# Performance work log

Measured on AMD Instinct MI355X. Metric: run time of the kernel, lower is better.

The kernel has to match this reference:

```python
import jax, jax.numpy as jnp
import numpy as np

EMBED = 1024
HEADS = 16
HEAD_DIM = EMBED // HEADS
FFN_DIM = 4096
SEQ = 2048
BATCH = 2
EPS = 1e-5


def setup_inputs() -> dict:
    key = jax.random.key(0)
    ks = jax.random.split(key, 13)
    s = lambda n: 1.0 / np.sqrt(n)
    return {
        "x": jax.random.normal(ks[0], (BATCH, SEQ, EMBED), jnp.float32),
        # qkv projection (stored as [in, out])
        "w_qkv": jax.random.normal(ks[1], (EMBED, 3 * EMBED), jnp.float32) * s(EMBED),
        "b_qkv": jax.random.normal(ks[2], (3 * EMBED,), jnp.float32) * 0.02,
        "w_out": jax.random.normal(ks[3], (EMBED, EMBED), jnp.float32) * s(EMBED),
        "b_out": jax.random.normal(ks[4], (EMBED,), jnp.float32) * 0.02,
        # FFN
        "w_up": jax.random.normal(ks[5], (EMBED, FFN_DIM), jnp.float32) * s(EMBED),
        "b_up": jax.random.normal(ks[6], (FFN_DIM,), jnp.float32) * 0.02,
        "w_down": jax.random.normal(ks[7], (FFN_DIM, EMBED), jnp.float32) * s(FFN_DIM),
        "b_down": jax.random.normal(ks[8], (EMBED,), jnp.float32) * 0.02,
        # LayerNorms
        "g1": jnp.ones((EMBED,), jnp.float32),
        "be1": jnp.zeros((EMBED,), jnp.float32),
        "g2": jnp.ones((EMBED,), jnp.float32),
        "be2": jnp.zeros((EMBED,), jnp.float32),
    }


def _layernorm(x, g, b):
    mu = jnp.mean(x, axis=-1, keepdims=True)
    var = jnp.mean(jnp.square(x - mu), axis=-1, keepdims=True)
    return (x - mu) * jax.lax.rsqrt(var + EPS) * g + b


def reference(x, w_qkv, b_qkv, w_out, b_out, w_up, b_up, w_down, b_down, g1, be1, g2, be2):
    B, S, E = x.shape
    qkv = (x @ w_qkv + b_qkv).reshape(B, S, 3, HEADS, HEAD_DIM)
    qkv = jnp.transpose(qkv, (2, 0, 3, 1, 4))
    q, k, v = qkv[0], qkv[1], qkv[2]
    scale = 1.0 / jnp.sqrt(jnp.float32(HEAD_DIM))
    attn = jnp.einsum("bhqd,bhkd->bhqk", q, k) * scale  # [B,H,S,S]
    causal = jnp.tril(jnp.ones((S, S), bool))
    attn = jnp.where(causal, attn, -jnp.inf)
    attn = jax.nn.softmax(attn, axis=-1)
    out = jnp.einsum("bhqk,bhkd->bhqd", attn, v)  # [B,H,S,D]
    out = jnp.transpose(out, (0, 2, 1, 3)).reshape(B, S, E)
    attn_out = out @ w_out + b_out
    x = _layernorm(x + attn_out, g1, be1)
    ffn_out = jax.nn.relu(x @ w_up + b_up) @ w_down + b_down
    return _layernorm(x + ffn_out, g2, be2)
```

## Files before the change

kernel.cpp:

```cpp
#include <hip/hip_runtime.h>
#include <hip/hip_bf16.h>

#define EMBED 1024
#define HEADS 16
#define HDIM 64
#define FFN 4096
#define SEQ 2048
#define BATCH 2
#define MTOT (BATCH*SEQ)
#define QSCALE 0.1803368801111137f

typedef __attribute__((ext_vector_type(8))) short bf16x8;
typedef __attribute__((ext_vector_type(4))) float f32x4;
typedef __attribute__((ext_vector_type(16))) float f32x16;
typedef unsigned short u16;
typedef unsigned int u32;

__device__ __forceinline__ u16 f2bf(float f) {
  union { float f; unsigned u; } v; v.f = f;
  unsigned r = v.u + 0x7FFFu + ((v.u >> 16) & 1u);
  return (u16)(r >> 16);
}

__device__ __forceinline__ void async_ld16(const void* g, void* l) {
  __builtin_amdgcn_global_load_lds((const __attribute__((address_space(1))) void*)g,
                                   (__attribute__((address_space(3))) void*)l,
                                   16, 0, 0);
}

__device__ __forceinline__ void qkv_scatter(u16* qp, u16* kp, u16* vp,
                                            int row, int col, float v) {
  const int which = col >> 10, hh = (col >> 6) & 15, d = col & 63;
  const int bb = row >> 11, ss = row & 2047;
  const int bh = bb * 16 + hh;
  if (which == 0) {
    v *= QSCALE;
    size_t idx = ((((size_t)bh * 64 + (ss >> 5)) * 4 + (d >> 4)) << 9)
               + (((ss & 31) + 32 * ((d >> 3) & 1)) << 3) + (d & 7);
    qp[idx] = f2bf(v);
  } else if (which == 1) {
    size_t idx = ((((size_t)bh * 32 + (ss >> 6)) * 8 + (d >> 4) * 2 + ((ss >> 5) & 1)) << 9)
               + (((ss & 31) + 32 * ((d >> 3) & 1)) << 3) + (d & 7);
    kp[idx] = f2bf(v);
  } else {
    size_t idx = ((((size_t)bh * 32 + (ss >> 6)) * 8 + ((ss & 63) >> 4) * 2 + (d >> 5)) << 9)
               + (((d & 31) + 32 * ((ss >> 3) & 1)) << 3) + (ss & 7);
    vp[idx] = f2bf(v);
  }
}

__global__ __launch_bounds__(256) void k_cvt(const float* __restrict__ in,
                                             u16* __restrict__ out, int n4) {
  int i = blockIdx.x * 256 + threadIdx.x;
  int st = gridDim.x * 256;
  for (; i < n4; i += st) {
    float4 v = ((const float4*)in)[i];
    ushort4 o;
    o.x = f2bf(v.x); o.y = f2bf(v.y); o.z = f2bf(v.z); o.w = f2bf(v.w);
    ((ushort4*)out)[i] = o;
  }
}

__global__ __launch_bounds__(256) void k_tr(const float* __restrict__ w,
                                            u16* __restrict__ wT, int K, int N) {
  __shared__ u16 tile[32][33];
  int n0 = blockIdx.x * 32, k0 = blockIdx.y * 32;
  int tx = threadIdx.x, ty = threadIdx.y;
  #pragma unroll
  for (int i = 0; i < 4; ++i) {
    int k = k0 + ty + i * 8;
    tile[ty + i * 8][tx] = f2bf(w[(size_t)k * N + n0 + tx]);
  }
  __syncthreads();
  #pragma unroll
  for (int i = 0; i < 4; ++i) {
    int n = n0 + ty + i * 8;
    wT[(size_t)n * K + k0 + tx] = tile[tx][ty + i * 8];
  }
}

template <int OMODE, bool RELU>
__global__ __launch_bounds__(512) void k_gemm8(
    const u16* __restrict__ A, const u16* __restrict__ BT,
    const float* __restrict__ bias,
    void* __restrict__ out0, void* __restrict__ out1, void* __restrict__ out2,
    int M, int N, int K) {
  __shared__ __align__(16) u16 As[2][2][128 * 64];
  __shared__ __align__(16) u16 Bs[2][2][128 * 64];
  const int tid = threadIdx.x;
  const int lane = tid & 63, g = lane >> 4, li = lane & 15;
  const int wid = tid >> 6, wm = wid >> 2, wn = wid & 3;

  const int gx = gridDim.x;
  const int nwg = gx * gridDim.y;
  const int flat = blockIdx.y * gx + blockIdx.x;
  const int cpx = nwg >> 3;
  const int swz = (flat & 7) * cpx + (flat >> 3);
  const int m0 = (swz / gx) * 256, n0 = (swz % gx) * 256;

  f32x4 acc[8][4] = {};

  const u16* Ablk = A + (size_t)m0 * K;
  const u16* Bblk = BT + (size_t)n0 * K;
  const int trow = tid >> 3;
  const int sc = (tid & 7) ^ (trow & 7);

  auto stageA = [&](int buf, int h, int kt) {
    #pragma unroll
    for (int r = 0; r < 2; ++r)
      async_ld16(Ablk + (size_t)(h * 64 + r * 128 + trow) * K + kt + sc * 8,
                 &As[buf][h][0] + r * 4096 + tid * 8);
  };
  auto stageB = [&](int buf, int h, int kt) {
    #pragma unroll
    for (int r = 0; r < 2; ++r) {
      const int p = trow + r * 64;
      async_ld16(Bblk + (size_t)(((p >> 5) << 6) + h * 32 + (p & 31)) * K + kt + sc * 8,
                 &Bs[buf][h][0] + r * 4096 + tid * 8);
    }
  };

#define VM4_ asm volatile("s_waitcnt vmcnt(4)" ::: "memory")
#define VM2_ asm volatile("s_waitcnt vmcnt(2)" ::: "memory")
#define VM0_ asm volatile("s_waitcnt vmcnt(0)" ::: "memory")
#define VMN_
#define GP8(IH, JH, VMSTMT, STAGE_STMT) do {                                   \
    bf16x8 a_[4][2], b_[2][2];                                                 \
    _Pragma("unroll")                                                          \
    for (int i2 = 0; i2 < 4; ++i2) {                                           \
      const int pa = wm * 64 + i2 * 16 + li;                                   \
      _Pragma("unroll")                                                        \
      for (int ks = 0; ks < 2; ++ks)                                           \
        a_[i2][ks] = *(const bf16x8*)(&As[cur][IH][0] + pa * 64 +              \
                                      (((ks * 4 + g) ^ (li & 7)) * 8));        \
    }                                                                          \
    _Pragma("unroll")                                                          \
    for (int j2 = 0; j2 < 2; ++j2) {                                           \
      const int pb = wn * 32 + j2 * 16 + li;                                   \
      _Pragma("unroll")                                                        \
      for (int ks = 0; ks < 2; ++ks)                                           \
        b_[j2][ks] = *(const bf16x8*)(&Bs[cur][JH][0] + pb * 64 +              \
                                      (((ks * 4 + g) ^ (li & 7)) * 8));        \
    }                                                                          \
    STAGE_STMT;                                                                \
    VMSTMT;                                                                    \
    __builtin_amdgcn_s_barrier();                                              \
    asm volatile("s_waitcnt lgkmcnt(0)" ::: "memory");                         \
    __builtin_amdgcn_sched_barrier(0);                                         \
    __builtin_amdgcn_s_setprio(1);                                             \
    _Pragma("unroll")                                                          \
    for (int ks = 0; ks < 2; ++ks)                                             \
      _Pragma("unroll")                                                        \
      for (int i2 = 0; i2 < 4; ++i2)                                           \
        _Pragma("unroll")                                                      \
        for (int j2 = 0; j2 < 2; ++j2)                                         \
          acc[IH * 4 + i2][JH * 2 + j2] = __builtin_amdgcn_mfma_f32_16x16x32_bf16( \
              a_[i2][ks], b_[j2][ks], acc[IH * 4 + i2][JH * 2 + j2], 0, 0, 0); \
    __builtin_amdgcn_s_setprio(0);                                             \
    __builtin_amdgcn_s_barrier();                                              \
    asm volatile("" ::: "memory");                                             \
  } while (0)

  stageA(0, 0, 0); stageB(0, 0, 0); stageA(0, 1, 0); stageB(0, 1, 0);
  VM4_;
  __builtin_amdgcn_s_barrier();
  asm volatile("" ::: "memory");

  int cur = 0;
  const int nkt = K >> 6;
  for (int t = 0; t < nkt - 1; ++t) {
    const int kn = (t + 1) * 64;
    GP8(0, 0, VM4_, stageA(cur ^ 1, 0, kn));
    GP8(1, 0, VM4_, stageB(cur ^ 1, 0, kn));
    GP8(0, 1, VMN_, stageA(cur ^ 1, 1, kn));
    GP8(1, 1, VM4_, stageB(cur ^ 1, 1, kn));
    cur ^= 1;
  }
  GP8(0, 0, VM2_, );
  GP8(1, 0, VM0_, );
  GP8(0, 1, VMN_, );
  GP8(1, 1, VMN_, );
#undef GP8
#undef VM4_
#undef VM2_
#undef VM0_
#undef VMN_

  float bcol[4];
  #pragma unroll
  for (int j = 0; j < 4; ++j) bcol[j] = bias[n0 + wn * 64 + j * 16 + li];

  #pragma unroll
  for (int i = 0; i < 8; ++i) {
    #pragma unroll
    for (int j = 0; j < 4; ++j) {
      #pragma unroll
      for (int r = 0; r < 4; ++r) {
        int row = m0 + wm * 128 + i * 16 + g * 4 + r;
        int col = n0 + wn * 64 + j * 16 + li;
        float v = acc[i][j][r] + bcol[j];
        if (RELU) v = fmaxf(v, 0.f);
        if (OMODE == 0) {
          ((u16*)out0)[(size_t)row * N + col] = f2bf(v);
        } else {
          qkv_scatter((u16*)out0, (u16*)out1, (u16*)out2, row, col, v);
        }
      }
    }
  }
}

template <bool RELU>
__global__ __launch_bounds__(256) void k_gemm3(
    const u16* __restrict__ A, const u16* __restrict__ BT,
    const float* __restrict__ bias, float* __restrict__ out,
    int M, int N, int K) {
  __shared__ __align__(16) u16 As[4][128 * 32];
  __shared__ __align__(16) u16 Bs[4][128 * 32];
  const int tid = threadIdx.x;
  const int lane = tid & 63, g = lane >> 4, li = lane & 15;
  const int wid = tid >> 6, wm = wid >> 1, wn = wid & 1;

  const int gx = gridDim.x;
  const int nwg = gx * gridDim.y;
  const int flat = blockIdx.y * gx + blockIdx.x;
  const int cpx = nwg >> 3;
  const int swz = (flat & 7) * cpx + (flat >> 3);
  const int m0 = (swz / gx) * 128, n0 = (swz % gx) * 128;

  f32x4 acc[4][4] = {};

  const u16* Ablk = A + (size_t)m0 * K;
  const u16* Bblk = BT + (size_t)n0 * K;
  const int trow = tid >> 2;
  const int sc = ((tid & 3) ^ (trow & 3)) * 8;

  auto stage = [&](int buf, int kt) {
    #pragma unroll
    for (int r = 0; r < 2; ++r) {
      async_ld16(Ablk + (size_t)(trow + r * 64) * K + kt + sc,
                 &As[buf][0] + r * 2048 + tid * 8);
      async_ld16(Bblk + (size_t)(trow + r * 64) * K + kt + sc,
                 &Bs[buf][0] + r * 2048 + tid * 8);
    }
  };

#define GM_VM8 asm volatile("s_waitcnt vmcnt(8)" ::: "memory")
#define GM_VM4 asm volatile("s_waitcnt vmcnt(4)" ::: "memory")
#define GM_VM0 asm volatile("s_waitcnt vmcnt(0)" ::: "memory")

  stage(0, 0); stage(1, 32); stage(2, 64);
  GM_VM8;
  __builtin_amdgcn_s_barrier();
  asm volatile("" ::: "memory");

  int cur = 0;
  for (int kt = 0; kt < K; kt += 32) {
    bf16x8 af[4], bfr[4];
    #pragma unroll
    for (int i = 0; i < 4; ++i) {
      const int row = wm * 64 + i * 16 + li;
      af[i] = *(const bf16x8*)(&As[cur][0] + row * 32 + ((g ^ (row & 3)) * 8));
    }
    #pragma unroll
    for (int j = 0; j < 4; ++j) {
      const int row = wn * 64 + j * 16 + li;
      bfr[j] = *(const bf16x8*)(&Bs[cur][0] + row * 32 + ((g ^ (row & 3)) * 8));
    }
    if (kt + 96 < K) stage((cur + 3) & 3, kt + 96);
    if (kt + 96 < K)      GM_VM8;
    else if (kt + 64 < K) GM_VM4;
    else if (kt + 32 < K) GM_VM0;
    __builtin_amdgcn_s_barrier();
    asm volatile("s_waitcnt lgkmcnt(0)" ::: "memory");
    __builtin_amdgcn_sched_barrier(0);
    __builtin_amdgcn_s_setprio(1);
    #pragma unroll
    for (int i = 0; i < 4; ++i)
      #pragma unroll
      for (int j = 0; j < 4; ++j)
        acc[i][j] = __builtin_amdgcn_mfma_f32_16x16x32_bf16(af[i], bfr[j], acc[i][j], 0, 0, 0);
    __builtin_amdgcn_s_setprio(0);
    __builtin_amdgcn_s_barrier();
    asm volatile("" ::: "memory");
    cur = (cur + 1) & 3;
  }
#undef GM_VM8
#undef GM_VM4
#undef GM_VM0

  float bcol[4];
  #pragma unroll
  for (int j = 0; j < 4; ++j) bcol[j] = bias[n0 + wn * 64 + j * 16 + li];

  #pragma unroll
  for (int i = 0; i < 4; ++i) {
    #pragma unroll
    for (int j = 0; j < 4; ++j) {
      #pragma unroll
      for (int r = 0; r < 4; ++r) {
        int row = m0 + wm * 64 + i * 16 + g * 4 + r;
        int col = n0 + wn * 64 + j * 16 + li;
        float v = acc[i][j][r] + bcol[j];
        if (RELU) v = fmaxf(v, 0.f);
        out[(size_t)row * N + col] = v;
      }
    }
  }
}

__global__ __launch_bounds__(256, 3) void k_attn7(
    const u16* __restrict__ Qp, const u16* __restrict__ Kp,
    const u16* __restrict__ Vp, u16* __restrict__ ctx) {
  const int bh = blockIdx.x;
  const int t32 = 63 - (int)blockIdx.y;
  const int b = bh >> 4, h = bh & 15;
  const int tid = threadIdx.x;
  const int wid = tid >> 6, lane = tid & 63;
  const int ql = lane & 31, hl = lane >> 5;

  __shared__ __align__(16) float mrg[3][64][34];

  const int wq0 = t32 * 32;
  const int qg = wq0 + ql;
  const int nt = ((wq0 + 31) >> 6) + 1;

  bf16x8 qf[4];
  {
    const u16* qpb = Qp + ((((size_t)bh * 64 + t32) * 4) << 9) + lane * 8;
    #pragma unroll
    for (int d4 = 0; d4 < 4; ++d4)
      qf[d4] = *(const bf16x8*)(qpb + (d4 << 9));
  }

  const u16* kbase = Kp + (((size_t)bh * 32) << 12) + lane * 8;
  const u16* vbase = Vp + (((size_t)bh * 32) << 12) + lane * 8;

  f32x16 o0 = {}, o1 = {};
  float m_run = -1e30f, l_run = 0.f;

  for (int kt = wid; kt < nt; kt += 4) {
    const bool kh1 = (kt * 64 + 32 <= wq0 + 31);
    const bool domask = (kt * 64 + (kh1 ? 63 : 31) > wq0);
    const u16* kb_ = kbase + ((size_t)kt << 12);
    const u16* vb_ = vbase + ((size_t)kt << 12);

    bf16x8 kf0[4], kf1[4];
    #pragma unroll
    for (int d4 = 0; d4 < 4; ++d4) {
      kf0[d4] = *(const bf16x8*)(kb_ + ((d4 * 2 + 0) << 9));
      if (kh1) kf1[d4] = *(const bf16x8*)(kb_ + ((d4 * 2 + 1) << 9));
    }
    bf16x8 vf0[4], vf1[4];
    #pragma unroll
    for (int t = 0; t < 4; ++t)
      if (t < 2 || kh1) {
        vf0[t] = *(const bf16x8*)(vb_ + ((t * 2 + 0) << 9));
        vf1[t] = *(const bf16x8*)(vb_ + ((t * 2 + 1) << 9));
      }

    f32x16 S0 = {}, S1 = {};
    #pragma unroll
    for (int d4 = 0; d4 < 4; ++d4)
      S0 = __builtin_amdgcn_mfma_f32_32x32x16_bf16(kf0[d4], qf[d4], S0, 0, 0, 0);
    if (kh1) {
      #pragma unroll
      for (int d4 = 0; d4 < 4; ++d4)
        S1 = __builtin_amdgcn_mfma_f32_32x32x16_bf16(kf1[d4], qf[d4], S1, 0, 0, 0);
    }

    if (domask) {
      const int qrel = qg - kt * 64 - 4 * hl;
      #pragma unroll
      for (int r = 0; r < 16; ++r) {
        const int kc = (r & 3) + 8 * (r >> 2);
        S0[r] = (kc <= qrel) ? S0[r] : -3.0e38f;
      }
      if (kh1) {
        #pragma unroll
        for (int r = 0; r < 16; ++r) {
          const int kc = 32 + (r & 3) + 8 * (r >> 2);
          S1[r] = (kc <= qrel) ? S1[r] : -3.0e38f;
        }
      }
    }

    float mt = -3.0e38f;
    #pragma unroll
    for (int r = 0; r < 16; ++r) mt = fmaxf(mt, S0[r]);
    if (kh1) {
      #pragma unroll
      for (int r = 0; r < 16; ++r) mt = fmaxf(mt, S1[r]);
    }
    mt = fmaxf(mt, __shfl_xor(mt, 32, 64));

    if (!__all(mt <= m_run + 8.0f)) {
      const float mn = fmaxf(m_run, mt);
      const float alpha = exp2f(m_run - mn);
      l_run *= alpha;
      o0 *= alpha;
      o1 *= alpha;
      m_run = mn;
    }
    float sum = 0.f;
    #pragma unroll
    for (int r = 0; r < 16; ++r) { S0[r] = exp2f(S0[r] - m_run); sum += S0[r]; }
    if (kh1) {
      #pragma unroll
      for (int r = 0; r < 16; ++r) { S1[r] = exp2f(S1[r] - m_run); sum += S1[r]; }
    }
    sum += __shfl_xor(sum, 32, 64);
    l_run += sum;

    u32 pk[2][8], sw[2][8];
    #pragma unroll
    for (int m = 0; m < 4; ++m) {
      asm("v_cvt_pk_bf16_f32 %0, %1, %2" : "=v"(pk[0][2*m])   : "v"(S0[4*m+0]), "v"(S0[4*m+1]));
      asm("v_cvt_pk_bf16_f32 %0, %1, %2" : "=v"(pk[0][2*m+1]) : "v"(S0[4*m+2]), "v"(S0[4*m+3]));
    }
    #pragma unroll
    for (int i = 0; i < 8; ++i) sw[0][i] = __shfl_xor(pk[0][i], 32, 64);
    if (kh1) {
      #pragma unroll
      for (int m = 0; m < 4; ++m) {
        asm("v_cvt_pk_bf16_f32 %0, %1, %2" : "=v"(pk[1][2*m])   : "v"(S1[4*m+0]), "v"(S1[4*m+1]));
        asm("v_cvt_pk_bf16_f32 %0, %1, %2" : "=v"(pk[1][2*m+1]) : "v"(S1[4*m+2]), "v"(S1[4*m+3]));
      }
      #pragma unroll
      for (int i = 0; i < 8; ++i) sw[1][i] = __shfl_xor(pk[1][i], 32, 64);
    }

    #pragma unroll
    for (int t = 0; t < 4; ++t) {
      if (t < 2 || kh1) {
        const int c = t >> 1, m0 = 2 * (t & 1), m1 = m0 + 1;
        union { u32 u[4]; bf16x8 v; } pf;
        pf.u[0] = hl ? sw[c][2*m1]   : pk[c][2*m0];
        pf.u[1] = hl ? sw[c][2*m1+1] : pk[c][2*m0+1];
        pf.u[2] = hl ? pk[c][2*m1]   : sw[c][2*m0];
        pf.u[3] = hl ? pk[c][2*m1+1] : sw[c][2*m0+1];
        o0 = __builtin_amdgcn_mfma_f32_32x32x16_bf16(vf0[t], pf.v, o0, 0, 0, 0);
        o1 = __builtin_amdgcn_mfma_f32_32x32x16_bf16(vf1[t], pf.v, o1, 0, 0, 0);
      }
    }
  }

  if (wid > 0) {
    float* p = &mrg[wid - 1][lane][0];
    *(f32x16*)(p) = o0;
    *(f32x16*)(p + 16) = o1;
    p[32] = m_run;
    p[33] = l_run;
  }
  __syncthreads();
  if (wid > 0) return;

  float M = m_run;
  #pragma unroll
  for (int w = 0; w < 3; ++w) M = fmaxf(M, mrg[w][lane][32]);
  const float fa = exp2f(m_run - M);
  f32x16 acc0 = o0 * fa, acc1 = o1 * fa;
  float L = l_run * fa;
  #pragma unroll
  for (int w = 0; w < 3; ++w) {
    const float* p = &mrg[w][lane][0];
    const float fw = exp2f(p[32] - M);
    L += p[33] * fw;
    f32x16 t0 = *(const f32x16*)(p);
    f32x16 t1 = *(const f32x16*)(p + 16);
    acc0 += t0 * fw;
    acc1 += t1 * fw;
  }
  const float inv = 1.f / L;

  u16* outp = ctx + (size_t)(b * SEQ + qg) * EMBED + h * HDIM + 4 * hl;
  #pragma unroll
  for (int m = 0; m < 4; ++m) {
    ushort4 s0v, s1v;
    s0v.x = f2bf(acc0[4*m+0] * inv); s0v.y = f2bf(acc0[4*m+1] * inv);
    s0v.z = f2bf(acc0[4*m+2] * inv); s0v.w = f2bf(acc0[4*m+3] * inv);
    *(ushort4*)(outp + 8 * m) = s0v;
    s1v.x = f2bf(acc1[4*m+0] * inv); s1v.y = f2bf(acc1[4*m+1] * inv);
    s1v.z = f2bf(acc1[4*m+2] * inv); s1v.w = f2bf(acc1[4*m+3] * inv);
    *(ushort4*)(outp + 32 + 8 * m) = s1v;
  }
}

__global__ __launch_bounds__(256) void k_add_ln(
    const float* __restrict__ a, const float* __restrict__ bmat,
    const float* __restrict__ gam, const float* __restrict__ bet,
    float* __restrict__ outf, u16* __restrict__ outb) {
  const int row = blockIdx.x;
  const int t = threadIdx.x;
  __shared__ float red[8];
  float4 va = ((const float4*)(a + (size_t)row * EMBED))[t];
  float4 vb = ((const float4*)(bmat + (size_t)row * EMBED))[t];
  float s0 = va.x + vb.x, s1 = va.y + vb.y, s2 = va.z + vb.z, s3 = va.w + vb.w;
  float sum = s0 + s1 + s2 + s3;
  float sq = s0 * s0 + s1 * s1 + s2 * s2 + s3 * s3;
  #pragma unroll
  for (int m = 1; m < 64; m <<= 1) {
    sum += __shfl_xor(sum, m, 64);
    sq += __shfl_xor(sq, m, 64);
  }
  int wid = t >> 6;
  if ((t & 63) == 0) { red[wid] = sum; red[4 + wid] = sq; }
  __syncthreads();
  sum = red[0] + red[1] + red[2] + red[3];
  sq = red[4] + red[5] + red[6] + red[7];
  float mean = sum * (1.f / EMBED);
  float var = sq * (1.f / EMBED) - mean * mean;
  float rstd = rsqrtf(var + 1e-5f);
  float4 gv = ((const float4*)gam)[t], bev = ((const float4*)bet)[t];
  float y0 = (s0 - mean) * rstd * gv.x + bev.x;
  float y1 = (s1 - mean) * rstd * gv.y + bev.y;
  float y2 = (s2 - mean) * rstd * gv.z + bev.z;
  float y3 = (s3 - mean) * rstd * gv.w + bev.w;
  if (outf) {
    float4 o; o.x = y0; o.y = y1; o.z = y2; o.w = y3;
    ((float4*)(outf + (size_t)row * EMBED))[t] = o;
  }
  if (outb) {
    ushort4 ob; ob.x = f2bf(y0); ob.y = f2bf(y1); ob.z = f2bf(y2); ob.w = f2bf(y3);
    ((ushort4*)(outb + (size_t)row * EMBED))[t] = ob;
  }
}

extern "C" void kernel_launch(void* const* d_in, const int* in_sizes, int n_in,
                              void* d_out, int out_size, void* d_ws, size_t ws_size,
                              hipStream_t stream) {
  const float* x      = (const float*)d_in[0];
  const float* w_qkv  = (const float*)d_in[1];
  const float* b_qkv  = (const float*)d_in[2];
  const float* w_out  = (const float*)d_in[3];
  const float* b_out  = (const float*)d_in[4];
  const float* w_up   = (const float*)d_in[5];
  const float* b_up   = (const float*)d_in[6];
  const float* w_down = (const float*)d_in[7];
  const float* b_down = (const float*)d_in[8];
  const float* g1  = (const float*)d_in[9];
  const float* be1 = (const float*)d_in[10];
  const float* g2  = (const float*)d_in[11];
  const float* be2 = (const float*)d_in[12];

  char* ws = (char*)d_ws;
  size_t off = 0;
  auto alloc = [&](size_t bytes) { void* p = ws + off; off += (bytes + 255) & ~(size_t)255; return p; };

  u16* xb     = (u16*)alloc((size_t)MTOT * EMBED * 2);
  u16* wqkvT  = (u16*)alloc((size_t)3 * EMBED * EMBED * 2);
  u16* woutT  = (u16*)alloc((size_t)EMBED * EMBED * 2);
  u16* wupT   = (u16*)alloc((size_t)FFN * EMBED * 2);
  u16* wdownT = (u16*)alloc((size_t)EMBED * FFN * 2);
  u16* qp     = (u16*)alloc((size_t)MTOT * EMBED * 2);
  u16* kp     = (u16*)alloc((size_t)MTOT * EMBED * 2);
  u16* vp     = (u16*)alloc((size_t)MTOT * EMBED * 2);
  u16* ctx    = (u16*)alloc((size_t)MTOT * EMBED * 2);
  float* attn_proj = (float*)alloc((size_t)MTOT * EMBED * 4);
  float* y_f32     = (float*)alloc((size_t)MTOT * EMBED * 4);
  u16* y_bf16      = (u16*)alloc((size_t)MTOT * EMBED * 2);
  u16* hmid        = (u16*)alloc((size_t)MTOT * FFN * 2);
  float* ffn_o     = (float*)alloc((size_t)MTOT * EMBED * 4);

  dim3 trb(32, 8);
  k_cvt<<<2048, 256, 0, stream>>>(x, xb, MTOT * EMBED / 4);
  k_tr<<<dim3(3 * EMBED / 32, EMBED / 32), trb, 0, stream>>>(w_qkv, wqkvT, EMBED, 3 * EMBED);
  k_tr<<<dim3(EMBED / 32, EMBED / 32), trb, 0, stream>>>(w_out, woutT, EMBED, EMBED);
  k_tr<<<dim3(FFN / 32, EMBED / 32), trb, 0, stream>>>(w_up, wupT, EMBED, FFN);
  k_tr<<<dim3(EMBED / 32, FFN / 32), trb, 0, stream>>>(w_down, wdownT, FFN, EMBED);

  k_gemm8<2, false><<<dim3(3 * EMBED / 256, MTOT / 256), 512, 0, stream>>>(
      xb, wqkvT, b_qkv, qp, kp, vp, MTOT, 3 * EMBED, EMBED);

  k_attn7<<<dim3(BATCH * HEADS, 64), 256, 0, stream>>>(qp, kp, vp, ctx);

  k_gemm3<false><<<dim3(EMBED / 128, MTOT / 128), 256, 0, stream>>>(
      ctx, woutT, b_out, attn_proj, MTOT, EMBED, EMBED);

  k_add_ln<<<MTOT, 256, 0, stream>>>(x, attn_proj, g1, be1, y_f32, y_bf16);

  k_gemm8<0, true><<<dim3(FFN / 256, MTOT / 256), 512, 0, stream>>>(
      y_bf16, wupT, b_up, hmid, nullptr, nullptr, MTOT, FFN, EMBED);

  k_gemm3<false><<<dim3(EMBED / 128, MTOT / 128), 256, 0, stream>>>(
      hmid, wdownT, b_down, ffn_o, MTOT, EMBED, FFN);

  k_add_ln<<<MTOT, 256, 0, stream>>>(y_f32, ffn_o, g2, be2, (float*)d_out, nullptr);

  (void)in_sizes; (void)n_in; (void)out_size; (void)ws_size;
}
```

Baseline: 242.5 us.

## Rework N=1024 GEMM into 8-wave 64-deep K pipeline with split A halves

Replaces the 4-wave 128x128 GEMM used for the output projection and FFN down-projection with an 8-wave version. It uses a 64-wide K tile with an XOR-swizzled shared layout and splits each stage into two A halves, so the second half's MFMAs overlap the remaining loads. The goal is more waves per block to hide latency and fewer, deeper K iterations to cut barrier overhead. In exchange the vmcnt gating becomes more intricate, and with fewer accumulators per wave the ratio of LDS reads to MFMAs changes.

```diff
diff --git a/kernel.cpp b/kernel.cpp
--- a/kernel.cpp
+++ b/kernel.cpp
@@ -211,15 +211,15 @@
 }
 
 template <bool RELU>
-__global__ __launch_bounds__(256) void k_gemm3(
+__global__ __launch_bounds__(512) void k_gemmD(
     const u16* __restrict__ A, const u16* __restrict__ BT,
     const float* __restrict__ bias, float* __restrict__ out,
     int M, int N, int K) {
-  __shared__ __align__(16) u16 As[4][128 * 32];
-  __shared__ __align__(16) u16 Bs[4][128 * 32];
+  __shared__ __align__(16) u16 As[4][2][64 * 64];
+  __shared__ __align__(16) u16 Bs[4][2][64 * 64];
   const int tid = threadIdx.x;
   const int lane = tid & 63, g = lane >> 4, li = lane & 15;
-  const int wid = tid >> 6, wm = wid >> 1, wn = wid & 1;
+  const int wid = tid >> 6, wm = wid >> 2, wn = wid & 3;
 
   const int gx = gridDim.x;
   const int nwg = gx * gridDim.y;
@@ -228,79 +228,112 @@
   const int swz = (flat & 7) * cpx + (flat >> 3);
   const int m0 = (swz / gx) * 128, n0 = (swz % gx) * 128;
 
-  f32x4 acc[4][4] = {};
+  f32x4 acc[4][2] = {};
 
   const u16* Ablk = A + (size_t)m0 * K;
   const u16* Bblk = BT + (size_t)n0 * K;
-  const int trow = tid >> 2;
-  const int sc = ((tid & 3) ^ (trow & 3)) * 8;
-
-  auto stage = [&](int buf, int kt) {
-    #pragma unroll
-    for (int r = 0; r < 2; ++r) {
-      async_ld16(Ablk + (size_t)(trow + r * 64) * K + kt + sc,
-                 &As[buf][0] + r * 2048 + tid * 8);
-      async_ld16(Bblk + (size_t)(trow + r * 64) * K + kt + sc,
-                 &Bs[buf][0] + r * 2048 + tid * 8);
+  const int p = tid >> 3;
+  const int c = (tid & 7) ^ (p & 7);
+
+  auto stageAll = [&](int buf, int kt) {
+    {
+      const int grow = (p >> 5) * 64 + 0 * 32 + (p & 31);
+      async_ld16(Ablk + (size_t)grow * K + kt + c * 8, &As[buf][0][0] + tid * 8);
+    }
+    {
+      const int grow = (p >> 4) * 32 + 0 * 16 + (p & 15);
+      async_ld16(Bblk + (size_t)grow * K + kt + c * 8, &Bs[buf][0][0] + tid * 8);
+    }
+    {
+      const int grow = (p >> 4) * 32 + 1 * 16 + (p & 15);
+      async_ld16(Bblk + (size_t)grow * K + kt + c * 8, &Bs[buf][1][0] + tid * 8);
+    }
+    {
+      const int grow = (p >> 5) * 64 + 1 * 32 + (p & 31);
+      async_ld16(Ablk + (size_t)grow * K + kt + c * 8, &As[buf][1][0] + tid * 8);
     }
   };
 
-#define GM_VM8 asm volatile("s_waitcnt vmcnt(8)" ::: "memory")
-#define GM_VM4 asm volatile("s_waitcnt vmcnt(4)" ::: "memory")
-#define GM_VM0 asm volatile("s_waitcnt vmcnt(0)" ::: "memory")
-
-  stage(0, 0); stage(1, 32); stage(2, 64);
-  GM_VM8;
+#define GATE(n) asm volatile("s_waitcnt vmcnt(" #n ")" ::: "memory")
+  stageAll(0, 0);
+  stageAll(1, 64);
+  GATE(5);
   __builtin_amdgcn_s_barrier();
   asm volatile("" ::: "memory");
 
-  int cur = 0;
-  for (int kt = 0; kt < K; kt += 32) {
-    bf16x8 af[4], bfr[4];
-    #pragma unroll
-    for (int i = 0; i < 4; ++i) {
-      const int row = wm * 64 + i * 16 + li;
-      af[i] = *(const bf16x8*)(&As[cur][0] + row * 32 + ((g ^ (row & 3)) * 8));
-    }
-    #pragma unroll
-    for (int j = 0; j < 4; ++j) {
-      const int row = wn * 64 + j * 16 + li;
-      bfr[j] = *(const bf16x8*)(&Bs[cur][0] + row * 32 + ((g ^ (row & 3)) * 8));
-    }
-    if (kt + 96 < K) stage((cur + 3) & 3, kt + 96);
-    if (kt + 96 < K)      GM_VM8;
-    else if (kt + 64 < K) GM_VM4;
-    else if (kt + 32 < K) GM_VM0;
+  const int nkt = K >> 6;
+  const int pa0 = wm * 32 + li, pa1 = wm * 32 + 16 + li;
+  const int pb = wn * 16 + li;
+  for (int t = 0; t < nkt; ++t) {
+    const int buf = t & 3;
+    bf16x8 a_[2][2], b_[2][2];
+    #pragma unroll
+    for (int ks = 0; ks < 2; ++ks) {
+      a_[0][ks] = *(const bf16x8*)(&As[buf][0][0] + pa0 * 64 + (((ks * 4 + g) ^ (pa0 & 7)) * 8));
+      a_[1][ks] = *(const bf16x8*)(&As[buf][0][0] + pa1 * 64 + (((ks * 4 + g) ^ (pa1 & 7)) * 8));
+      b_[0][ks] = *(const bf16x8*)(&Bs[buf][0][0] + pb * 64 + (((ks * 4 + g) ^ (pb & 7)) * 8));
+      b_[1][ks] = *(const bf16x8*)(&Bs[buf][1][0] + pb * 64 + (((ks * 4 + g) ^ (pb & 7)) * 8));
+    }
+    if (t + 2 < nkt) {
+      stageAll((t + 2) & 3, (t + 2) * 64);
+      GATE(8);
+    } else if (t + 1 < nkt) {
+      GATE(4);
+    } else {
+      GATE(0);
+    }
     __builtin_amdgcn_s_barrier();
     asm volatile("s_waitcnt lgkmcnt(0)" ::: "memory");
     __builtin_amdgcn_sched_barrier(0);
     __builtin_amdgcn_s_setprio(1);
     #pragma unroll
-    for (int i = 0; i < 4; ++i)
-      #pragma unroll
-      for (int j = 0; j < 4; ++j)
-        acc[i][j] = __builtin_amdgcn_mfma_f32_16x16x32_bf16(af[i], bfr[j], acc[i][j], 0, 0, 0);
+    for (int ks = 0; ks < 2; ++ks)
+      #pragma unroll
+      for (int i2l = 0; i2l < 2; ++i2l)
+        #pragma unroll
+        for (int j2 = 0; j2 < 2; ++j2)
+          acc[i2l][j2] = __builtin_amdgcn_mfma_f32_16x16x32_bf16(
+              a_[i2l][ks], b_[j2][ks], acc[i2l][j2], 0, 0, 0);
     __builtin_amdgcn_s_setprio(0);
     __builtin_amdgcn_s_barrier();
     asm volatile("" ::: "memory");
-    cur = (cur + 1) & 3;
-  }
-#undef GM_VM8
-#undef GM_VM4
-#undef GM_VM0
-
-  float bcol[4];
-  #pragma unroll
-  for (int j = 0; j < 4; ++j) bcol[j] = bias[n0 + wn * 64 + j * 16 + li];
+    #pragma unroll
+    for (int ks = 0; ks < 2; ++ks) {
+      a_[0][ks] = *(const bf16x8*)(&As[buf][1][0] + pa0 * 64 + (((ks * 4 + g) ^ (pa0 & 7)) * 8));
+      a_[1][ks] = *(const bf16x8*)(&As[buf][1][0] + pa1 * 64 + (((ks * 4 + g) ^ (pa1 & 7)) * 8));
+    }
+    if (t + 2 < nkt)      GATE(5);
+    else if (t + 1 < nkt) GATE(1);
+    __builtin_amdgcn_s_barrier();
+    asm volatile("s_waitcnt lgkmcnt(0)" ::: "memory");
+    __builtin_amdgcn_sched_barrier(0);
+    __builtin_amdgcn_s_setprio(1);
+    #pragma unroll
+    for (int ks = 0; ks < 2; ++ks)
+      #pragma unroll
+      for (int i2l = 0; i2l < 2; ++i2l)
+        #pragma unroll
+        for (int j2 = 0; j2 < 2; ++j2)
+          acc[2 + i2l][j2] = __builtin_amdgcn_mfma_f32_16x16x32_bf16(
+              a_[i2l][ks], b_[j2][ks], acc[2 + i2l][j2], 0, 0, 0);
+    __builtin_amdgcn_s_setprio(0);
+    __builtin_amdgcn_s_barrier();
+    asm volatile("" ::: "memory");
+  }
+#undef GATE
+
+  float bcol[2];
+  #pragma unroll
+  for (int j = 0; j < 2; ++j) bcol[j] = bias[n0 + wn * 32 + j * 16 + li];
 
   #pragma unroll
   for (int i = 0; i < 4; ++i) {
     #pragma unroll
-    for (int j = 0; j < 4; ++j) {
+    for (int j = 0; j < 2; ++j) {
       #pragma unroll
       for (int r = 0; r < 4; ++r) {
         int row = m0 + wm * 64 + i * 16 + g * 4 + r;
-        int col = n0 + wn * 64 + j * 16 + li;
+        int col = n0 + wn * 32 + j * 16 + li;
         float v = acc[i][j][r] + bcol[j];
         if (RELU) v = fmaxf(v, 0.f);
         out[(size_t)row * N + col] = v;
@@ -446,11 +479,11 @@
   }
 
   if (wid > 0) {
-    float* p = &mrg[wid - 1][lane][0];
-    *(f32x16*)(p) = o0;
-    *(f32x16*)(p + 16) = o1;
-    p[32] = m_run;
-    p[33] = l_run;
+    float* pq = &mrg[wid - 1][lane][0];
+    *(f32x16*)(pq) = o0;
+    *(f32x16*)(pq + 16) = o1;
+    pq[32] = m_run;
+    pq[33] = l_run;
   }
   __syncthreads();
   if (wid > 0) return;
@@ -463,11 +496,11 @@
   float L = l_run * fa;
   #pragma unroll
   for (int w = 0; w < 3; ++w) {
-    const float* p = &mrg[w][lane][0];
-    const float fw = exp2f(p[32] - M);
-    L += p[33] * fw;
-    f32x16 t0 = *(const f32x16*)(p);
-    f32x16 t1 = *(const f32x16*)(p + 16);
+    const float* pq = &mrg[w][lane][0];
+    const float fw = exp2f(pq[32] - M);
+    L += pq[33] * fw;
+    f32x16 t0 = *(const f32x16*)(pq);
+    f32x16 t1 = *(const f32x16*)(pq + 16);
     acc0 += t0 * fw;
     acc1 += t1 * fw;
   }
@@ -574,7 +607,7 @@
 
   k_attn7<<<dim3(BATCH * HEADS, 64), 256, 0, stream>>>(qp, kp, vp, ctx);
 
-  k_gemm3<false><<<dim3(EMBED / 128, MTOT / 128), 256, 0, stream>>>(
+  k_gemmD<false><<<dim3(EMBED / 128, MTOT / 128), 512, 0, stream>>>(
       ctx, woutT, b_out, attn_proj, MTOT, EMBED, EMBED);
 
   k_add_ln<<<MTOT, 256, 0, stream>>>(x, attn_proj, g1, be1, y_f32, y_bf16);
@@ -582,7 +615,7 @@
   k_gemm8<0, true><<<dim3(FFN / 256, MTOT / 256), 512, 0, stream>>>(
       y_bf16, wupT, b_up, hmid, nullptr, nullptr, MTOT, FFN, EMBED);
 
-  k_gemm3<false><<<dim3(EMBED / 128, MTOT / 128), 256, 0, stream>>>(
+  k_gemmD<false><<<dim3(EMBED / 128, MTOT / 128), 512, 0, stream>>>(
       hmid, wdownT, b_down, ffn_o, MTOT, EMBED, FFN);
 
   k_add_ln<<<MTOT, 256, 0, stream>>>(y_f32, ffn_o, g2, be2, (float*)d_out, nullptr);
```

Measured after the change: 246.9 us. Within noise of the previous version (+1.8%).
